# Kernel optimization log

Measured on AMD Instinct MI355X. Metric: run time of the kernel, lower is better.

Reference implementation:

```python
import jax, jax.numpy as jnp
import numpy as np

S = 8          # num_slots
DSLOT = 128    # slot_dim
D_IN = 768     # input feature dim
ITERS = 3      # slot_att_iter
RES = 21       # 336 // 16
NGRID = RES * RES   # 441 grid positions
NTOK = 441          # tokens kept per frame (no drop here)
NFRAME = 2
F_ = 2 * NFRAME + 1  # 5 frames per clip
CLIPS = 8
B = CLIPS * F_       # 40
SIGMA = 5.0
SCALE = DSLOT ** -0.5
EPS = 1e-8


def layernorm(x, g, b):
    m = x.mean(-1, keepdims=True)
    v = ((x - m) ** 2).mean(-1, keepdims=True)
    return (x - m) * jax.lax.rsqrt(v + 1e-5) * g + b


def setup_inputs() -> dict:
    key = jax.random.key(0)
    ks = iter(jax.random.split(key, 64))
    def nrm(shape, s=0.02):
        return jax.random.normal(next(ks), shape, jnp.float32) * s
    xs = jnp.linspace(-1.0, 1.0, RES)
    ys = jnp.linspace(-1.0, 1.0, RES)
    gx, gy = jnp.meshgrid(xs, ys)  # indexing='xy' as in torch
    abs_grid = jnp.stack([gx.ravel(), gy.ravel()], axis=-1)  # [NGRID, 2]
    return {
        "inputs": jax.random.normal(next(ks), (B, NTOK, D_IN), jnp.float32),
        "token_indices": jnp.sort(jax.random.randint(next(ks), (B, NTOK), 0, NGRID), axis=-1),
        "abs_grid": abs_grid,
        "slots_init": nrm((1, S, DSLOT), 0.1),
        "S_p_init": nrm((1, S, 1, 2), 0.02),
        "S_s_init": jax.random.uniform(next(ks), (1, S, 1, 2), jnp.float32, 0.3, 0.7),
        "WQ": nrm((DSLOT, DSLOT)), "ln_g": jnp.ones((DSLOT,)), "ln_b": jnp.zeros((DSLOT,)),
        "gru_w_ih": nrm((DSLOT, 3 * DSLOT)), "gru_w_hh": nrm((DSLOT, 3 * DSLOT)),
        "gru_b_ih": jnp.zeros((3 * DSLOT,)), "gru_b_hh": jnp.zeros((3 * DSLOT,)),
        "mlp_ln_g": jnp.ones((DSLOT,)), "mlp_ln_b": jnp.zeros((DSLOT,)),
        "mlp_w1": nrm((DSLOT, 4 * DSLOT)), "mlp_b1": jnp.zeros((4 * DSLOT,)),
        "mlp_w2": nrm((4 * DSLOT, DSLOT)), "mlp_b2": jnp.zeros((DSLOT,)),
        "WK": nrm((DSLOT, DSLOT)), "WV": nrm((DSLOT, DSLOT)),
        "Wg": nrm((2, DSLOT)), "bg": jnp.zeros((DSLOT,)),
        "Wf1": nrm((DSLOT, DSLOT)), "bf1": jnp.zeros((DSLOT,)),
        "Wf2": nrm((DSLOT, DSLOT)), "bf2": jnp.zeros((DSLOT,)),
        "im_ln1_g": jnp.ones((D_IN,)), "im_ln1_b": jnp.zeros((D_IN,)),
        "im_w1": nrm((D_IN, D_IN)), "im_b1": jnp.zeros((D_IN,)),
        "im_w2": nrm((D_IN, DSLOT)), "im_b2": jnp.zeros((DSLOT,)),
        "im_ln2_g": jnp.ones((DSLOT,)), "im_ln2_b": jnp.zeros((DSLOT,)),
        "fin_w": nrm((DSLOT, DSLOT)), "fin_b": jnp.zeros((DSLOT,)),
    }


def _forward(inputs, token_indices, abs_grid, slots_init, S_p_init, S_s_init,
             WQ, ln_g, ln_b, gru_w_ih, gru_w_hh, gru_b_ih, gru_b_hh,
             mlp_ln_g, mlp_ln_b, mlp_w1, mlp_b1, mlp_w2, mlp_b2,
             WK, WV, Wg, bg, Wf1, bf1, Wf2, bf2,
             im_ln1_g, im_ln1_b, im_w1, im_b1, im_w2, im_b2, im_ln2_g, im_ln2_b,
             fin_w, fin_b):
    Bb = inputs.shape[0]
    # initial_mlp: LN -> Linear -> ReLU -> Linear -> LN
    x = layernorm(inputs, im_ln1_g, im_ln1_b)
    x = jax.nn.relu(x @ im_w1 + im_b1)
    x = x @ im_w2 + im_b2
    x = layernorm(x, im_ln2_g, im_ln2_b)          # [B, N, Dslot]
    # K/V projections of inputs are slot-independent; compute once.
    Kx = x @ WK                                    # [B, N, Dslot]
    Vx = x @ WV
    ag = abs_grid[token_indices]                   # [B, N, 2] per-batch gather
    slots = jnp.broadcast_to(slots_init, (Bb, S, DSLOT))
    S_p = jnp.broadcast_to(S_p_init, (Bb, S, 1, 2))
    S_s = jnp.broadcast_to(S_s_init, (Bb, S, 1, 2))

    def f_net(z):  # f = Linear -> ReLU -> Linear
        return jax.nn.relu(z @ Wf1 + bf1) @ Wf2 + bf2

    attn = None
    for t in range(ITERS + 1):
        slots_prev = slots
        sn = layernorm(slots, ln_g, ln_b)
        rel = (ag[:, None] - S_p) / (S_s * SIGMA)  # [B, S, N, 2]
        gr = rel @ Wg + bg                          # [B, S, N, Dslot]
        k = f_net(Kx[:, None] + gr)
        v = f_net(Vx[:, None] + gr)
        q = sn @ WQ                                 # [B, S, Dslot]
        dots = jnp.einsum('bsd,bsjd->bsj', q, k) * SCALE
        attn = jax.nn.softmax(dots, axis=1) + EPS   # softmax over slots
        attn = attn / attn.sum(-1, keepdims=True)   # renormalize over tokens
        updates = jnp.einsum('bsjd,bsj->bsd', v, attn)
        S_p = jnp.einsum('bjd,bsj->bsd', ag, attn)[:, :, None, :]
        S_s = jnp.sqrt(jnp.einsum('bsjd,bsj->bsd', (ag[:, None] - S_p) ** 2, attn))[:, :, None, :]
        if t != ITERS:
            # torch GRUCell
            xg = updates.reshape(-1, DSLOT)
            hg = slots_prev.reshape(-1, DSLOT)
            gi = xg @ gru_w_ih + gru_b_ih
            gh = hg @ gru_w_hh + gru_b_hh
            i_r, i_z, i_n = jnp.split(gi, 3, axis=-1)
            h_r, h_z, h_n = jnp.split(gh, 3, axis=-1)
            r = jax.nn.sigmoid(i_r + h_r)
            z = jax.nn.sigmoid(i_z + h_z)
            n = jnp.tanh(i_n + r * h_n)
            slots = ((1.0 - z) * n + z * hg).reshape(Bb, S, DSLOT)
            # residual pre-LN MLP (dropout is identity in eval)
            y = layernorm(slots, mlp_ln_g, mlp_ln_b)
            y = jax.nn.relu(y @ mlp_w1 + mlp_b1) @ mlp_w2 + mlp_b2
            slots = slots + y
    slots = slots @ fin_w + fin_b
    attn_out = attn.reshape(-1, F_, S, NTOK)[:, NFRAME]  # center frame
    return slots, attn_out


def reference(inputs, token_indices, abs_grid, slots_init, S_p_init, S_s_init,
              WQ, ln_g, ln_b, gru_w_ih, gru_w_hh, gru_b_ih, gru_b_hh,
              mlp_ln_g, mlp_ln_b, mlp_w1, mlp_b1, mlp_w2, mlp_b2,
              WK, WV, Wg, bg, Wf1, bf1, Wf2, bf2,
              im_ln1_g, im_ln1_b, im_w1, im_b1, im_w2, im_b2, im_ln2_g, im_ln2_b,
              fin_w, fin_b):
    return _forward(inputs, token_indices, abs_grid, slots_init, S_p_init, S_s_init,
                    WQ, ln_g, ln_b, gru_w_ih, gru_w_hh, gru_b_ih, gru_b_hh,
                    mlp_ln_g, mlp_ln_b, mlp_w1, mlp_b1, mlp_w2, mlp_b2,
                    WK, WV, Wg, bg, Wf1, bf1, Wf2, bf2,
                    im_ln1_g, im_ln1_b, im_w1, im_b1, im_w2, im_b2, im_ln2_g, im_ln2_b,
                    fin_w, fin_b)
```

## Files before the change

### kernel.cpp

```cpp
#include <hip/hip_runtime.h>
#include <cstdio>

#define NB 40
#define NS 8
#define NT 441
#define DIN 768
#define DD 128
#define NTOT (NB*NT)
#define FSCALE 0.08838834764831843f

typedef short s8v __attribute__((ext_vector_type(8)));
typedef float f4v __attribute__((ext_vector_type(4)));

__device__ inline ushort f2bf(float f){
  unsigned u = __float_as_uint(f);
  unsigned r = (u + 0x7fffu + ((u >> 16) & 1u)) >> 16;
  return (ushort)r;
}
__device__ inline float bf2f(ushort h){ return __uint_as_float(((unsigned)h) << 16); }

struct PP {
  const float *inputs; const int *tok_idx; const float *abs_grid;
  const float *slots_init, *Sp_init, *Ss_init;
  const float *WQ, *ln_g, *ln_b;
  const float *gru_w_ih, *gru_w_hh, *gru_b_ih, *gru_b_hh;
  const float *mlp_ln_g, *mlp_ln_b, *mlp_w1, *mlp_b1, *mlp_w2, *mlp_b2;
  const float *WK, *WV, *Wg, *bg, *Wf1, *bf1, *Wf2, *bf2;
  const float *im_ln1_g, *im_ln1_b, *im_w1, *im_b1, *im_w2, *im_b2, *im_ln2_g, *im_ln2_b;
  const float *fin_w, *fin_b;
  float *x, *A_K, *A_V, *ag, *WKf, *WVf, *Wg1, *c1, *Wf2T;
  float *slots, *Sp0, *Sp1, *Ss0, *Ss1, *qW, *qb, *dots, *attn;
  float *hbar_part, *Sp_part, *hbar;
  ushort *xnh, *xnl, *hh, *hl, *W1Th, *W1Tl, *W2Th, *W2Tl;
  float *out;
};

__global__ __launch_bounds__(128) void prep_weights(PP p){
  int r = blockIdx.x, d = threadIdx.x;
  float accK = 0.f, accV = 0.f;
  for (int kk = 0; kk < DD; kk++){
    float w = p.Wf1[kk*DD + d];
    accK = fmaf(p.WK[r*DD+kk], w, accK);
    accV = fmaf(p.WV[r*DD+kk], w, accV);
  }
  p.WKf[r*DD+d] = accK; p.WVf[r*DD+d] = accV;
  if (r < 2){
    float a = 0.f;
    for (int kk = 0; kk < DD; kk++) a = fmaf(p.Wg[r*DD+kk], p.Wf1[kk*DD+d], a);
    p.Wg1[r*DD+d] = a;
  }
  if (r == 2){
    float a = 0.f;
    for (int kk = 0; kk < DD; kk++) a = fmaf(p.bg[kk], p.Wf1[kk*DD+d], a);
    p.c1[d] = a + p.bf1[d];
  }
  p.Wf2T[d*DD + r] = p.Wf2[r*DD + d];
}

__global__ __launch_bounds__(256) void transpose_split(const float* __restrict__ W,
                                                       ushort* __restrict__ WTh,
                                                       ushort* __restrict__ WTl,
                                                       int K, int N){
  __shared__ float tile[64][65];
  int tid = threadIdx.x;
  int k0 = blockIdx.x * 64, n0 = blockIdx.y * 64;
  #pragma unroll
  for (int i = 0; i < 4; i++){
    int k = i*16 + (tid >> 4);
    int n4 = (tid & 15) * 4;
    float4 v = *(const float4*)(W + (long)(k0+k)*N + n0 + n4);
    tile[k][n4+0] = v.x; tile[k][n4+1] = v.y; tile[k][n4+2] = v.z; tile[k][n4+3] = v.w;
  }
  __syncthreads();
  #pragma unroll
  for (int i = 0; i < 4; i++){
    int n = i*16 + (tid >> 4);
    int k4 = (tid & 15) * 4;
    ushort4 h4, l4;
    float v0 = tile[k4+0][n], v1 = tile[k4+1][n], v2 = tile[k4+2][n], v3 = tile[k4+3][n];
    h4.x = f2bf(v0); l4.x = f2bf(v0 - bf2f(h4.x));
    h4.y = f2bf(v1); l4.y = f2bf(v1 - bf2f(h4.y));
    h4.z = f2bf(v2); l4.z = f2bf(v2 - bf2f(h4.z));
    h4.w = f2bf(v3); l4.w = f2bf(v3 - bf2f(h4.w));
    *(ushort4*)(WTh + (long)(n0+n)*K + k0 + k4) = h4;
    *(ushort4*)(WTl + (long)(n0+n)*K + k0 + k4) = l4;
  }
}

__global__ __launch_bounds__(256) void ln1_split(PP p){
  int tok = blockIdx.x*4 + (threadIdx.x >> 6);
  int l = threadIdx.x & 63;
  const float* src = p.inputs + (long)tok*DIN;
  float4 v[3];
  float s = 0.f, s2 = 0.f;
  #pragma unroll
  for (int pp = 0; pp < 3; pp++){
    v[pp] = *(const float4*)(src + pp*256 + l*4);
    s  += v[pp].x + v[pp].y + v[pp].z + v[pp].w;
    s2 += v[pp].x*v[pp].x + v[pp].y*v[pp].y + v[pp].z*v[pp].z + v[pp].w*v[pp].w;
  }
  #pragma unroll
  for (int m = 1; m < 64; m <<= 1){ s += __shfl_xor(s, m); s2 += __shfl_xor(s2, m); }
  float mean = s*(1.f/DIN), var = s2*(1.f/DIN) - mean*mean;
  float rstd = rsqrtf(var + 1e-5f);
  #pragma unroll
  for (int pp = 0; pp < 3; pp++){
    int idx = pp*256 + l*4;
    float4 g = *(const float4*)(p.im_ln1_g + idx);
    float4 b = *(const float4*)(p.im_ln1_b + idx);
    float y0 = (v[pp].x-mean)*rstd*g.x + b.x;
    float y1 = (v[pp].y-mean)*rstd*g.y + b.y;
    float y2 = (v[pp].z-mean)*rstd*g.z + b.z;
    float y3 = (v[pp].w-mean)*rstd*g.w + b.w;
    ushort4 h4, l4;
    h4.x = f2bf(y0); l4.x = f2bf(y0 - bf2f(h4.x));
    h4.y = f2bf(y1); l4.y = f2bf(y1 - bf2f(h4.y));
    h4.z = f2bf(y2); l4.z = f2bf(y2 - bf2f(h4.z));
    h4.w = f2bf(y3); l4.w = f2bf(y3 - bf2f(h4.w));
    *(ushort4*)(p.xnh + (long)tok*DIN + idx) = h4;
    *(ushort4*)(p.xnl + (long)tok*DIN + idx) = l4;
  }
}

template<int EPI>
__global__ __launch_bounds__(256) void gemm_split(
    const ushort* __restrict__ Ah, const ushort* __restrict__ Al,
    const ushort* __restrict__ Bh, const ushort* __restrict__ Bl,
    const float* __restrict__ bias,
    ushort* __restrict__ Ch, ushort* __restrict__ Cl,
    float* __restrict__ Xout, const float* __restrict__ g2, const float* __restrict__ b2,
    int M)
{
  __shared__ __align__(16) char smem[64*132*4];
  ushort* As = (ushort*)smem;
  ushort* Bs = (ushort*)(smem + 10240);
  int tid = threadIdx.x;
  int n0 = blockIdx.x * 128, m0 = blockIdx.y * 64;
  int w = tid >> 6, lane = tid & 63;
  f4v acc[4][2];
  #pragma unroll
  for (int mf = 0; mf < 4; mf++)
    #pragma unroll
    for (int nf = 0; nf < 2; nf++) acc[mf][nf] = (f4v)(0.f);

  for (int kb = 0; kb < DIN; kb += 32){
    __syncthreads();
    #pragma unroll
    for (int i = 0; i < 2; i++){
      int c = tid + i*256;
      int s = c >> 8, r = (c >> 2) & 63, kg = c & 3;
      int gr = min(m0 + r, M-1);
      const float4 va = *(const float4*)((s ? Al : Ah) + (long)gr*DIN + kb + kg*8);
      *(float4*)(As + s*2560 + r*40 + kg*8) = va;
    }
    #pragma unroll
    for (int i = 0; i < 4; i++){
      int c = tid + i*256;
      int s = c >> 9, r = (c >> 2) & 127, kg = c & 3;
      const float4 vb = *(const float4*)((s ? Bl : Bh) + (long)(n0 + r)*DIN + kb + kg*8);
      *(float4*)(Bs + s*5120 + r*40 + kg*8) = vb;
    }
    __syncthreads();
    int kg = lane >> 4, rA = lane & 15;
    s8v a0[4], a1[4], b0[2], b1[2];
    #pragma unroll
    for (int mf = 0; mf < 4; mf++){
      a0[mf] = *(const s8v*)(As +        (mf*16 + rA)*40 + kg*8);
      a1[mf] = *(const s8v*)(As + 2560 + (mf*16 + rA)*40 + kg*8);
    }
    #pragma unroll
    for (int nf = 0; nf < 2; nf++){
      int rb = w*32 + nf*16 + rA;
      b0[nf] = *(const s8v*)(Bs +        rb*40 + kg*8);
      b1[nf] = *(const s8v*)(Bs + 5120 + rb*40 + kg*8);
    }
    #pragma unroll
    for (int mf = 0; mf < 4; mf++)
      #pragma unroll
      for (int nf = 0; nf < 2; nf++){
        acc[mf][nf] = __builtin_amdgcn_mfma_f32_16x16x32_bf16(a0[mf], b0[nf], acc[mf][nf], 0, 0, 0);
        acc[mf][nf] = __builtin_amdgcn_mfma_f32_16x16x32_bf16(a0[mf], b1[nf], acc[mf][nf], 0, 0, 0);
        acc[mf][nf] = __builtin_amdgcn_mfma_f32_16x16x32_bf16(a1[mf], b0[nf], acc[mf][nf], 0, 0, 0);
      }
  }

  int rbase = (lane >> 4) * 4, cn = lane & 15;
  if (EPI == 1){
    #pragma unroll
    for (int mf = 0; mf < 4; mf++)
      #pragma unroll
      for (int nf = 0; nf < 2; nf++){
        int n = n0 + w*32 + nf*16 + cn;
        float bs = bias[n];
        #pragma unroll
        for (int r = 0; r < 4; r++){
          int m = m0 + mf*16 + rbase + r;
          if (m < M){
            float v = fmaxf(acc[mf][nf][r] + bs, 0.f);
            ushort h = f2bf(v);
            Ch[(long)m*DIN + n] = h;
            Cl[(long)m*DIN + n] = f2bf(v - bf2f(h));
          }
        }
      }
  } else {
    __syncthreads();
    float* Dl = (float*)smem;
    #pragma unroll
    for (int mf = 0; mf < 4; mf++)
      #pragma unroll
      for (int nf = 0; nf < 2; nf++){
        int n = w*32 + nf*16 + cn;
        float bs = bias[n];
        #pragma unroll
        for (int r = 0; r < 4; r++)
          Dl[(mf*16 + rbase + r)*132 + n] = acc[mf][nf][r] + bs;
      }
    __syncthreads();
    for (int rr = 0; rr < 16; rr++){
      int row = w*16 + rr;
      float e0 = Dl[row*132 + lane], e1 = Dl[row*132 + 64 + lane];
      float s = e0 + e1, s2 = e0*e0 + e1*e1;
      #pragma unroll
      for (int m2 = 1; m2 < 64; m2 <<= 1){ s += __shfl_xor(s, m2); s2 += __shfl_xor(s2, m2); }
      float mean = s*(1.f/DD), var = s2*(1.f/DD) - mean*mean;
      float rstd = rsqrtf(var + 1e-5f);
      int m = m0 + row;
      if (m < M){
        Xout[(long)m*DD + lane]      = (e0-mean)*rstd*g2[lane]      + b2[lane];
        Xout[(long)m*DD + 64 + lane] = (e1-mean)*rstd*g2[64 + lane] + b2[64 + lane];
      }
    }
  }
}

__global__ void init_state(PP p){
  int i = blockIdx.x*256 + threadIdx.x;
  if (i < NB*NS*DD) p.slots[i] = p.slots_init[i & (NS*DD-1)];
  if (i < NB*NS*2){
    p.Sp0[i] = p.Sp_init[i & (NS*2-1)];
    p.Ss0[i] = p.Ss_init[i & (NS*2-1)];
  }
}

__global__ void gather_ag(PP p){
  int i = blockIdx.x*256 + threadIdx.x;
  if (i < NTOT){
    int idx = p.tok_idx[i];
    p.ag[i*2+0] = p.abs_grid[idx*2+0];
    p.ag[i*2+1] = p.abs_grid[idx*2+1];
  }
}

__global__ __launch_bounds__(256) void k2_proj(PP p){
  __shared__ float xt[32][132];
  int tid = threadIdx.x; int g0 = blockIdx.x * 32;
  for (int f = tid; f < 32*32; f += 256){
    int tok = f >> 5, pos = (f & 31) * 4;
    int gt = g0 + tok;
    float4 v = (gt < NTOT) ? *(const float4*)(p.x + (long)gt*DD + pos)
                           : make_float4(0.f,0.f,0.f,0.f);
    *(float4*)&xt[tok][pos] = v;
  }
  __syncthreads();
  int d = tid & 127, grp = tid >> 7;
  float aK[16], aV[16];
  float c1v = p.c1[d];
  #pragma unroll
  for (int t = 0; t < 16; t++){ aK[t] = c1v; aV[t] = c1v; }
  for (int kk = 0; kk < DD; kk += 4){
    float k0 = p.WKf[(kk+0)*DD+d], k1 = p.WKf[(kk+1)*DD+d], k2 = p.WKf[(kk+2)*DD+d], k3 = p.WKf[(kk+3)*DD+d];
    float v0 = p.WVf[(kk+0)*DD+d], v1 = p.WVf[(kk+1)*DD+d], v2 = p.WVf[(kk+2)*DD+d], v3 = p.WVf[(kk+3)*DD+d];
    #pragma unroll
    for (int t = 0; t < 16; t++){
      float4 xv = *(const float4*)&xt[grp*16+t][kk];
      aK[t] = fmaf(xv.x,k0, fmaf(xv.y,k1, fmaf(xv.z,k2, fmaf(xv.w,k3, aK[t]))));
      aV[t] = fmaf(xv.x,v0, fmaf(xv.y,v1, fmaf(xv.z,v2, fmaf(xv.w,v3, aV[t]))));
    }
  }
  #pragma unroll
  for (int t = 0; t < 16; t++){
    int gt = g0 + grp*16 + t;
    if (gt < NTOT){ p.A_K[(long)gt*DD+d] = aK[t]; p.A_V[(long)gt*DD+d] = aV[t]; }
  }
}

__global__ __launch_bounds__(128) void k3_slots(PP p){
  int bs = blockIdx.x, d = threadIdx.x;
  __shared__ float sn[128], q[128];
  __shared__ float rs[2][2];
  float v = p.slots[bs*DD+d];
  float s = v, s2 = v*v;
  for (int m = 1; m < 64; m <<= 1){ s += __shfl_xor(s, m); s2 += __shfl_xor(s2, m); }
  if ((d & 63) == 0){ rs[d>>6][0] = s; rs[d>>6][1] = s2; }
  __syncthreads();
  s = rs[0][0] + rs[1][0]; s2 = rs[0][1] + rs[1][1];
  float mean = s*(1.f/DD), var = s2*(1.f/DD) - mean*mean, rstd = rsqrtf(var + 1e-5f);
  sn[d] = (v-mean)*rstd*p.ln_g[d] + p.ln_b[d];
  __syncthreads();
  float acc = 0.f;
  for (int kk = 0; kk < DD; kk++) acc = fmaf(sn[kk], p.WQ[kk*DD+d], acc);
  q[d] = acc;
  __syncthreads();
  float a2 = 0.f;
  for (int dd = 0; dd < DD; dd++) a2 = fmaf(q[dd], p.Wf2T[dd*DD+d], a2);
  p.qW[bs*DD+d] = a2;
  float pb = p.bf2[d]*q[d];
  for (int m = 1; m < 64; m <<= 1) pb += __shfl_xor(pb, m);
  if ((d & 63) == 0) rs[d>>6][0] = pb;
  __syncthreads();
  if (d == 0) p.qb[bs] = (rs[0][0] + rs[1][0]) * FSCALE;
}

__global__ __launch_bounds__(256) void k4_dots(PP p, const float* Sp, const float* Ss){
  int b = blockIdx.x / 7, tile = blockIdx.x % 7;
  int tid = threadIdx.x, wid = tid >> 6, lane = tid & 63;
  int tl = lane >> 2, dg = lane & 3;
  __shared__ float qws[8][132];
  __shared__ float spss[8][4];
  __shared__ float qbs[8];
  for (int f = tid; f < 8*128; f += 256){
    int s = f >> 7, d = f & 127;
    qws[s][(d&31)*4 + (d>>5)] = p.qW[(b*NS+s)*DD+d];
  }
  if (tid < 8) qbs[tid] = p.qb[b*NS+tid];
  if (tid < 32){
    int s = tid >> 2, c = tid & 3;
    spss[s][c] = (c < 2) ? Sp[(b*NS+s)*2+c] : 1.f/(Ss[(b*NS+s)*2+(c-2)]*5.0f);
  }
  __syncthreads();
  int j = tile*64 + wid*16 + tl;
  bool valid = j < NT;
  int jj = valid ? j : 0;
  float aa[32], w0[32], w1[32];
  {
    const float* src = p.A_K + ((long)(b*NT+jj))*DD + dg*32;
    #pragma unroll
    for (int i4 = 0; i4 < 8; i4++){
      float4 t = *(const float4*)(src + i4*4);
      aa[i4*4+0]=t.x; aa[i4*4+1]=t.y; aa[i4*4+2]=t.z; aa[i4*4+3]=t.w;
    }
    #pragma unroll
    for (int i4 = 0; i4 < 8; i4++){
      float4 t0 = *(const float4*)(p.Wg1 + dg*32 + i4*4);
      float4 t1 = *(const float4*)(p.Wg1 + DD + dg*32 + i4*4);
      w0[i4*4+0]=t0.x; w0[i4*4+1]=t0.y; w0[i4*4+2]=t0.z; w0[i4*4+3]=t0.w;
      w1[i4*4+0]=t1.x; w1[i4*4+1]=t1.y; w1[i4*4+2]=t1.z; w1[i4*4+3]=t1.w;
    }
  }
  float ag0 = p.ag[(b*NT+jj)*2], ag1 = p.ag[(b*NT+jj)*2+1];
  #pragma unroll
  for (int s = 0; s < 8; s++){
    float rel0 = (ag0 - spss[s][0])*spss[s][2];
    float rel1 = (ag1 - spss[s][1])*spss[s][3];
    float acc = 0.f;
    #pragma unroll
    for (int i = 0; i < 32; i++){
      float hk = fmaxf(fmaf(rel0, w0[i], fmaf(rel1, w1[i], aa[i])), 0.f);
      acc = fmaf(hk, qws[s][i*4+dg], acc);
    }
    acc += __shfl_xor(acc, 1); acc += __shfl_xor(acc, 2);
    if (dg == 0 && valid) p.dots[(b*NS+s)*NT + j] = acc*FSCALE + qbs[s];
  }
}

__global__ __launch_bounds__(256) void k5_softmax(PP p){
  int b = blockIdx.x, tid = threadIdx.x;
  float a0[8], a1[8];
  float psum[8];
  #pragma unroll
  for (int s = 0; s < 8; s++) psum[s] = 0.f;
  bool has1 = (tid + 256) < NT;
  {
    int j = tid;
    float dv[8]; float m = -1e30f;
    #pragma unroll
    for (int s = 0; s < 8; s++){ dv[s] = p.dots[(b*NS+s)*NT+j]; m = fmaxf(m, dv[s]); }
    float tot = 0.f;
    #pragma unroll
    for (int s = 0; s < 8; s++){ dv[s] = expf(dv[s]-m); tot += dv[s]; }
    float inv = 1.f/tot;
    #pragma unroll
    for (int s = 0; s < 8; s++){ a0[s] = dv[s]*inv + 1e-8f; psum[s] += a0[s]; }
  }
  if (has1){
    int j = tid + 256;
    float dv[8]; float m = -1e30f;
    #pragma unroll
    for (int s = 0; s < 8; s++){ dv[s] = p.dots[(b*NS+s)*NT+j]; m = fmaxf(m, dv[s]); }
    float tot = 0.f;
    #pragma unroll
    for (int s = 0; s < 8; s++){ dv[s] = expf(dv[s]-m); tot += dv[s]; }
    float inv = 1.f/tot;
    #pragma unroll
    for (int s = 0; s < 8; s++){ a1[s] = dv[s]*inv + 1e-8f; psum[s] += a1[s]; }
  }
  #pragma unroll
  for (int s = 0; s < 8; s++)
    for (int m2 = 1; m2 < 64; m2 <<= 1) psum[s] += __shfl_xor(psum[s], m2);
  __shared__ float wsum[4][8];
  __shared__ float sums[8];
  if ((tid & 63) == 0)
    for (int s = 0; s < 8; s++) wsum[tid>>6][s] = psum[s];
  __syncthreads();
  if (tid < 8) sums[tid] = wsum[0][tid]+wsum[1][tid]+wsum[2][tid]+wsum[3][tid];
  __syncthreads();
  {
    int j = tid;
    #pragma unroll
    for (int s = 0; s < 8; s++) p.attn[(b*NS+s)*NT+j] = a0[s]/sums[s];
  }
  if (has1){
    int j = tid + 256;
    #pragma unroll
    for (int s = 0; s < 8; s++) p.attn[(b*NS+s)*NT+j] = a1[s]/sums[s];
  }
}

__global__ __launch_bounds__(256) void k6a(PP p, const float* Sp, const float* Ss){
  int b = blockIdx.x >> 3, tile = blockIdx.x & 7;
  int tid = threadIdx.x, wid = tid >> 6, lane = tid & 63;
  int j0 = tile*56; int jn = min(NT, j0+56) - j0;
  __shared__ float atile[8][56];
  __shared__ float spss[8][4];
  __shared__ float hpart[4][8][128];
  __shared__ float ppart[4][8][2];
  for (int f = tid; f < 8*56; f += 256){
    int s = f/56, jj = f%56;
    atile[s][jj] = (j0+jj < NT) ? p.attn[(b*NS+s)*NT + j0+jj] : 0.f;
  }
  if (tid < 32){
    int s = tid >> 2, c = tid & 3;
    spss[s][c] = (c < 2) ? Sp[(b*NS+s)*2+c] : 1.f/(Ss[(b*NS+s)*2+(c-2)]*5.0f);
  }
  __syncthreads();
  int d0 = lane, d1 = lane + 64;
  float wg00 = p.Wg1[d0], wg10 = p.Wg1[DD+d0], wg01 = p.Wg1[d1], wg11 = p.Wg1[DD+d1];
  float acc0[8], acc1[8], accp[8];
  #pragma unroll
  for (int s = 0; s < 8; s++){ acc0[s]=0.f; acc1[s]=0.f; accp[s]=0.f; }
  int cpar = lane & 1;
  for (int jj = wid; jj < jn; jj += 4){
    int j = j0 + jj;
    float av0 = p.A_V[((long)(b*NT+j))*DD + d0];
    float av1 = p.A_V[((long)(b*NT+j))*DD + d1];
    float ag0 = p.ag[(b*NT+j)*2], ag1 = p.ag[(b*NT+j)*2+1];
    float agc = cpar ? ag1 : ag0;
    #pragma unroll
    for (int s = 0; s < 8; s++){
      float rel0 = (ag0 - spss[s][0])*spss[s][2];
      float rel1 = (ag1 - spss[s][1])*spss[s][3];
      float a = atile[s][jj];
      float hv0 = fmaxf(fmaf(rel0,wg00, fmaf(rel1,wg10, av0)), 0.f);
      float hv1 = fmaxf(fmaf(rel0,wg01, fmaf(rel1,wg11, av1)), 0.f);
      acc0[s] = fmaf(a, hv0, acc0[s]);
      acc1[s] = fmaf(a, hv1, acc1[s]);
      if (lane < 2) accp[s] = fmaf(a, agc, accp[s]);
    }
  }
  #pragma unroll
  for (int s = 0; s < 8; s++){ hpart[wid][s][d0] = acc0[s]; hpart[wid][s][d1] = acc1[s]; }
  if (lane < 2)
    for (int s = 0; s < 8; s++) ppart[wid][s][lane] = accp[s];
  __syncthreads();
  for (int f = tid; f < 8*128; f += 256){
    int s = f >> 7, d = f & 127;
    p.hbar_part[((b*8+tile)*NS+s)*DD+d] = hpart[0][s][d]+hpart[1][s][d]+hpart[2][s][d]+hpart[3][s][d];
  }
  if (tid < 16){
    int s = tid >> 1, c = tid & 1;
    p.Sp_part[((b*8+tile)*NS+s)*2+c] = ppart[0][s][c]+ppart[1][s][c]+ppart[2][s][c]+ppart[3][s][c];
  }
}

__global__ __launch_bounds__(128) void k6r(PP p, float* Sp_new, float* Ss_new){
  int bs = blockIdx.x; int b = bs >> 3, s = bs & 7, d = threadIdx.x;
  float v = 0.f;
  for (int t = 0; t < 8; t++) v += p.hbar_part[((b*8+t)*NS+s)*DD+d];
  p.hbar[bs*DD+d] = v;
  __shared__ float spl[2];
  if (d < 2){
    float u = 0.f;
    for (int t = 0; t < 8; t++) u += p.Sp_part[((b*8+t)*NS+s)*2+d];
    Sp_new[bs*2+d] = u; spl[d] = u;
  }
  __syncthreads();
  float sp0 = spl[0], sp1 = spl[1];
  float q0 = 0.f, q1 = 0.f;
  for (int j = d; j < NT; j += 128){
    float at = p.attn[bs*NT+j];
    float e0 = p.ag[(b*NT+j)*2]   - sp0;
    float e1 = p.ag[(b*NT+j)*2+1] - sp1;
    q0 = fmaf(at, e0*e0, q0); q1 = fmaf(at, e1*e1, q1);
  }
  for (int m = 1; m < 64; m <<= 1){ q0 += __shfl_xor(q0, m); q1 += __shfl_xor(q1, m); }
  __shared__ float rr[2][2];
  if ((d & 63) == 0){ rr[d>>6][0] = q0; rr[d>>6][1] = q1; }
  __syncthreads();
  if (d == 0){
    Ss_new[bs*2+0] = sqrtf(rr[0][0]+rr[1][0]);
    Ss_new[bs*2+1] = sqrtf(rr[0][1]+rr[1][1]);
  }
}

__global__ __launch_bounds__(128) void k7_update(PP p){
  int bs = blockIdx.x, d = threadIdx.x;
  __shared__ float hb[128], upd[128], hprev[128], y[128], h1[512];
  __shared__ float rr[2][2];
  hb[d] = p.hbar[bs*DD+d]; hprev[d] = p.slots[bs*DD+d];
  __syncthreads();
  float a = p.bf2[d];
  for (int kk = 0; kk < DD; kk++) a = fmaf(hb[kk], p.Wf2[kk*DD+d], a);
  upd[d] = a;
  __syncthreads();
  float gi[3], gh[3];
  #pragma unroll
  for (int i = 0; i < 3; i++){ gi[i] = p.gru_b_ih[d+128*i]; gh[i] = p.gru_b_hh[d+128*i]; }
  for (int kk = 0; kk < DD; kk++){
    float xv = upd[kk], hv = hprev[kk];
    #pragma unroll
    for (int i = 0; i < 3; i++){
      gi[i] = fmaf(xv, p.gru_w_ih[kk*384 + d+128*i], gi[i]);
      gh[i] = fmaf(hv, p.gru_w_hh[kk*384 + d+128*i], gh[i]);
    }
  }
  float r = 1.f/(1.f+expf(-(gi[0]+gh[0])));
  float z = 1.f/(1.f+expf(-(gi[1]+gh[1])));
  float n = tanhf(gi[2] + r*gh[2]);
  float hnew = (1.f-z)*n + z*hprev[d];
  float s = hnew, s2 = hnew*hnew;
  for (int m = 1; m < 64; m <<= 1){ s += __shfl_xor(s, m); s2 += __shfl_xor(s2, m); }
  if ((d & 63) == 0){ rr[d>>6][0] = s; rr[d>>6][1] = s2; }
  __syncthreads();
  s = rr[0][0]+rr[1][0]; s2 = rr[0][1]+rr[1][1];
  float mean = s*(1.f/DD), var = s2*(1.f/DD)-mean*mean, rstd = rsqrtf(var+1e-5f);
  y[d] = (hnew-mean)*rstd*p.mlp_ln_g[d] + p.mlp_ln_b[d];
  __syncthreads();
  #pragma unroll
  for (int i = 0; i < 4; i++){
    int o = d + 128*i;
    float acc = p.mlp_b1[o];
    for (int kk = 0; kk < DD; kk++) acc = fmaf(y[kk], p.mlp_w1[kk*512+o], acc);
    h1[o] = fmaxf(acc, 0.f);
  }
  __syncthreads();
  float acc2 = p.mlp_b2[d];
  for (int o = 0; o < 512; o++) acc2 = fmaf(h1[o], p.mlp_w2[o*DD+d], acc2);
  p.slots[bs*DD+d] = hnew + acc2;
}

__global__ __launch_bounds__(128) void k8_final(PP p){
  int bs = blockIdx.x, d = threadIdx.x;
  __shared__ float sl[128];
  sl[d] = p.slots[bs*DD+d];
  __syncthreads();
  float a = p.fin_b[d];
  for (int kk = 0; kk < DD; kk++) a = fmaf(sl[kk], p.fin_w[kk*DD+d], a);
  p.out[bs*DD+d] = a;
}

__global__ void k8_attn(PP p){
  int i = blockIdx.x*256 + threadIdx.x;
  if (i < 8*NS*NT){
    int clip = i / (NS*NT);
    int rem  = i % (NS*NT);
    int b = clip*5 + 2;
    p.out[NB*NS*DD + i] = p.attn[b*NS*NT + rem];
  }
}

extern "C" void kernel_launch(void* const* d_in, const int* in_sizes, int n_in,
                              void* d_out, int out_size, void* d_ws, size_t ws_size,
                              hipStream_t stream){
  PP p;
  p.inputs=(const float*)d_in[0]; p.tok_idx=(const int*)d_in[1]; p.abs_grid=(const float*)d_in[2];
  p.slots_init=(const float*)d_in[3]; p.Sp_init=(const float*)d_in[4]; p.Ss_init=(const float*)d_in[5];
  p.WQ=(const float*)d_in[6]; p.ln_g=(const float*)d_in[7]; p.ln_b=(const float*)d_in[8];
  p.gru_w_ih=(const float*)d_in[9]; p.gru_w_hh=(const float*)d_in[10];
  p.gru_b_ih=(const float*)d_in[11]; p.gru_b_hh=(const float*)d_in[12];
  p.mlp_ln_g=(const float*)d_in[13]; p.mlp_ln_b=(const float*)d_in[14];
  p.mlp_w1=(const float*)d_in[15]; p.mlp_b1=(const float*)d_in[16];
  p.mlp_w2=(const float*)d_in[17]; p.mlp_b2=(const float*)d_in[18];
  p.WK=(const float*)d_in[19]; p.WV=(const float*)d_in[20]; p.Wg=(const float*)d_in[21]; p.bg=(const float*)d_in[22];
  p.Wf1=(const float*)d_in[23]; p.bf1=(const float*)d_in[24]; p.Wf2=(const float*)d_in[25]; p.bf2=(const float*)d_in[26];
  p.im_ln1_g=(const float*)d_in[27]; p.im_ln1_b=(const float*)d_in[28];
  p.im_w1=(const float*)d_in[29]; p.im_b1=(const float*)d_in[30];
  p.im_w2=(const float*)d_in[31]; p.im_b2=(const float*)d_in[32];
  p.im_ln2_g=(const float*)d_in[33]; p.im_ln2_b=(const float*)d_in[34];
  p.fin_w=(const float*)d_in[35]; p.fin_b=(const float*)d_in[36];

  float* w = (float*)d_ws;
  size_t need = 0;
  auto alloc = [&](size_t nfl){ nfl = (nfl + 3) & ~(size_t)3; float* r = w + need; need += nfl; return r; };
  p.x    = alloc((size_t)NTOT*DD);
  p.A_K  = alloc((size_t)NTOT*DD);
  p.A_V  = alloc((size_t)NTOT*DD);
  p.ag   = alloc((size_t)NTOT*2);
  p.WKf  = alloc(DD*DD);
  p.WVf  = alloc(DD*DD);
  p.Wg1  = alloc(2*DD);
  p.c1   = alloc(DD);
  p.Wf2T = alloc(DD*DD);
  p.slots= alloc(NB*NS*DD);
  p.Sp0  = alloc(NB*NS*2);
  p.Sp1  = alloc(NB*NS*2);
  p.Ss0  = alloc(NB*NS*2);
  p.Ss1  = alloc(NB*NS*2);
  p.qW   = alloc(NB*NS*DD);
  p.qb   = alloc(NB*NS);
  p.dots = alloc((size_t)NB*NS*NT);
  p.attn = alloc((size_t)NB*NS*NT);
  p.hbar_part = alloc((size_t)NB*8*NS*DD);
  p.Sp_part   = alloc((size_t)NB*8*NS*2);
  p.hbar = alloc(NB*NS*DD);
  p.xnh  = (ushort*)alloc((size_t)NTOT*DIN/2);
  p.xnl  = (ushort*)alloc((size_t)NTOT*DIN/2);
  p.hh   = (ushort*)alloc((size_t)NTOT*DIN/2);
  p.hl   = (ushort*)alloc((size_t)NTOT*DIN/2);
  p.W1Th = (ushort*)alloc((size_t)DIN*DIN/2);
  p.W1Tl = (ushort*)alloc((size_t)DIN*DIN/2);
  p.W2Th = (ushort*)alloc((size_t)DD*DIN/2);
  p.W2Tl = (ushort*)alloc((size_t)DD*DIN/2);
  p.out = (float*)d_out;
  if (ws_size < need*sizeof(float)){
    fprintf(stderr, "kernel_launch: ws too small (%zu < %zu)\n", ws_size, need*sizeof(float));
    return;
  }

  prep_weights<<<dim3(DD), dim3(DD), 0, stream>>>(p);
  transpose_split<<<dim3(DIN/64, DIN/64), dim3(256), 0, stream>>>(p.im_w1, p.W1Th, p.W1Tl, DIN, DIN);
  transpose_split<<<dim3(DIN/64, DD/64), dim3(256), 0, stream>>>(p.im_w2, p.W2Th, p.W2Tl, DIN, DD);
  init_state<<<dim3((NB*NS*DD+255)/256), dim3(256), 0, stream>>>(p);
  gather_ag<<<dim3((NTOT+255)/256), dim3(256), 0, stream>>>(p);
  ln1_split<<<dim3(NTOT/4), dim3(256), 0, stream>>>(p);
  gemm_split<1><<<dim3(DIN/128, (NTOT+63)/64), dim3(256), 0, stream>>>(
      p.xnh, p.xnl, p.W1Th, p.W1Tl, p.im_b1, p.hh, p.hl,
      nullptr, nullptr, nullptr, NTOT);
  gemm_split<2><<<dim3(1, (NTOT+63)/64), dim3(256), 0, stream>>>(
      p.hh, p.hl, p.W2Th, p.W2Tl, p.im_b2, nullptr, nullptr,
      p.x, p.im_ln2_g, p.im_ln2_b, NTOT);
  k2_proj<<<dim3((NTOT+31)/32), dim3(256), 0, stream>>>(p);

  float* Sp[2] = {p.Sp0, p.Sp1};
  float* Ss[2] = {p.Ss0, p.Ss1};
  int cur = 0;
  for (int t = 0; t < 4; t++){
    k3_slots<<<dim3(NB*NS), dim3(128), 0, stream>>>(p);
    k4_dots<<<dim3(NB*7), dim3(256), 0, stream>>>(p, Sp[cur], Ss[cur]);
    k5_softmax<<<dim3(NB), dim3(256), 0, stream>>>(p);
    if (t < 3){
      k6a<<<dim3(NB*8), dim3(256), 0, stream>>>(p, Sp[cur], Ss[cur]);
      k6r<<<dim3(NB*NS), dim3(128), 0, stream>>>(p, Sp[cur^1], Ss[cur^1]);
      k7_update<<<dim3(NB*NS), dim3(128), 0, stream>>>(p);
      cur ^= 1;
    }
  }
  k8_final<<<dim3(NB*NS), dim3(128), 0, stream>>>(p);
  k8_attn<<<dim3((8*NS*NT+255)/256), dim3(256), 0, stream>>>(p);
}
```

Baseline: 477.3 us.

## Fuse slot-attention iteration loop into one persistent per-batch kernel

Replaces the roughly 20 small per-iteration launches (slot LN/query, dots, softmax, weighted aggregation, reductions, GRU/MLP update, final projection) with a single kernel of one 512-thread block per batch element. All iteration state stays in shared memory, and the token grid gather and state init are folded in. Weight matrices are pre-transposed so each lane reads contiguous float4 rows. This removes launch overhead and global round-trips of intermediates, but only 40 blocks run on a large GPU, so per-batch work is serialized within one CU.

```diff
diff --git a/kernel.cpp b/kernel.cpp
--- a/kernel.cpp
+++ b/kernel.cpp
@@ -4,6 +4,7 @@
 #define NB 40
 #define NS 8
 #define NT 441
+#define NTP 448
 #define DIN 768
 #define DD 128
 #define NTOT (NB*NT)
@@ -18,6 +19,9 @@
   return (ushort)r;
 }
 __device__ inline float bf2f(ushort h){ return __uint_as_float(((unsigned)h) << 16); }
+__device__ inline float dot4(float4 a, float4 b){
+  return fmaf(a.x,b.x, fmaf(a.y,b.y, fmaf(a.z,b.z, a.w*b.w)));
+}
 
 struct PP {
   const float *inputs; const int *tok_idx; const float *abs_grid;
@@ -28,9 +32,8 @@
   const float *WK, *WV, *Wg, *bg, *Wf1, *bf1, *Wf2, *bf2;
   const float *im_ln1_g, *im_ln1_b, *im_w1, *im_b1, *im_w2, *im_b2, *im_ln2_g, *im_ln2_b;
   const float *fin_w, *fin_b;
-  float *x, *A_K, *A_V, *ag, *WKf, *WVf, *Wg1, *c1, *Wf2T;
-  float *slots, *Sp0, *Sp1, *Ss0, *Ss1, *qW, *qb, *dots, *attn;
-  float *hbar_part, *Sp_part, *hbar;
+  float *x, *A_K, *A_V, *WKf, *WVf, *Wg1, *c1, *Wf2T;
+  float *WQT, *gihT, *ghhT, *w1T, *w2T, *finT;
   ushort *xnh, *xnl, *hh, *hl, *W1Th, *W1Tl, *W2Th, *W2Tl;
   float *out;
 };
@@ -55,6 +58,21 @@
     p.c1[d] = a + p.bf1[d];
   }
   p.Wf2T[d*DD + r] = p.Wf2[r*DD + d];
+}
+
+__global__ __launch_bounds__(256) void prep_transposes(PP p){
+  long i = (long)blockIdx.x*256 + threadIdx.x;
+  if (i < 16384){ int r = i >> 7, c = i & 127; p.WQT[c*128 + r] = p.WQ[i]; return; }
+  i -= 16384;
+  if (i < 49152){ int r = i / 384, c = i % 384; p.gihT[c*128 + r] = p.gru_w_ih[i]; return; }
+  i -= 49152;
+  if (i < 49152){ int r = i / 384, c = i % 384; p.ghhT[c*128 + r] = p.gru_w_hh[i]; return; }
+  i -= 49152;
+  if (i < 65536){ int r = i / 512, c = i % 512; p.w1T[c*128 + r] = p.mlp_w1[i]; return; }
+  i -= 65536;
+  if (i < 65536){ int r = i / 128, c = i % 128; p.w2T[c*512 + r] = p.mlp_w2[i]; return; }
+  i -= 65536;
+  { int r = i >> 7, c = i & 127; p.finT[c*128 + r] = p.fin_w[i]; }
 }
 
 __global__ __launch_bounds__(256) void transpose_split(const float* __restrict__ W,
@@ -234,24 +252,6 @@
   }
 }
 
-__global__ void init_state(PP p){
-  int i = blockIdx.x*256 + threadIdx.x;
-  if (i < NB*NS*DD) p.slots[i] = p.slots_init[i & (NS*DD-1)];
-  if (i < NB*NS*2){
-    p.Sp0[i] = p.Sp_init[i & (NS*2-1)];
-    p.Ss0[i] = p.Ss_init[i & (NS*2-1)];
-  }
-}
-
-__global__ void gather_ag(PP p){
-  int i = blockIdx.x*256 + threadIdx.x;
-  if (i < NTOT){
-    int idx = p.tok_idx[i];
-    p.ag[i*2+0] = p.abs_grid[idx*2+0];
-    p.ag[i*2+1] = p.abs_grid[idx*2+1];
-  }
-}
-
 __global__ __launch_bounds__(256) void k2_proj(PP p){
   __shared__ float xt[32][132];
   int tid = threadIdx.x; int g0 = blockIdx.x * 32;
@@ -285,287 +285,333 @@
   }
 }
 
-__global__ __launch_bounds__(128) void k3_slots(PP p){
-  int bs = blockIdx.x, d = threadIdx.x;
-  __shared__ float sn[128], q[128];
-  __shared__ float rs[2][2];
-  float v = p.slots[bs*DD+d];
-  float s = v, s2 = v*v;
-  for (int m = 1; m < 64; m <<= 1){ s += __shfl_xor(s, m); s2 += __shfl_xor(s2, m); }
-  if ((d & 63) == 0){ rs[d>>6][0] = s; rs[d>>6][1] = s2; }
+__global__ __launch_bounds__(512) void k_iter(PP p){
+  const int b = blockIdx.x;
+  const int tid = threadIdx.x;
+  const int wid = tid >> 6, lane = tid & 63;
+
+  __shared__ float slots_s[8][128];
+  __shared__ float sns[8][128];
+  __shared__ float qs[8][128];
+  __shared__ float ys[8][128];
+  __shared__ float hbar_s[8][128];
+  __shared__ float upds[8][128];
+  __shared__ float qws[8][132];
+  __shared__ float qbs[8];
+  __shared__ float spss[8][4];
+  __shared__ float Sp_c[8][2], Ss_c[8][2];
+  __shared__ float agl[NTP][2];
+  __shared__ float wg01[2][128];
+  __shared__ float red[8][16];
+  __shared__ float sums[8];
+  __shared__ float u_a[4096];
+  __shared__ float u_b[4096];
+
+  for (int f = tid; f < NS*DD; f += 512) slots_s[f>>7][f&127] = p.slots_init[f];
+  if (tid < 16){ Sp_c[tid>>1][tid&1] = p.Sp_init[tid]; Ss_c[tid>>1][tid&1] = p.Ss_init[tid]; }
+  for (int f = tid; f < NT; f += 512){
+    int idx = p.tok_idx[b*NT + f];
+    agl[f][0] = p.abs_grid[idx*2+0];
+    agl[f][1] = p.abs_grid[idx*2+1];
+  }
+  if (tid < 256) wg01[tid>>7][tid&127] = p.Wg1[tid];
   __syncthreads();
-  s = rs[0][0] + rs[1][0]; s2 = rs[0][1] + rs[1][1];
-  float mean = s*(1.f/DD), var = s2*(1.f/DD) - mean*mean, rstd = rsqrtf(var + 1e-5f);
-  sn[d] = (v-mean)*rstd*p.ln_g[d] + p.ln_b[d];
-  __syncthreads();
-  float acc = 0.f;
-  for (int kk = 0; kk < DD; kk++) acc = fmaf(sn[kk], p.WQ[kk*DD+d], acc);
-  q[d] = acc;
-  __syncthreads();
-  float a2 = 0.f;
-  for (int dd = 0; dd < DD; dd++) a2 = fmaf(q[dd], p.Wf2T[dd*DD+d], a2);
-  p.qW[bs*DD+d] = a2;
-  float pb = p.bf2[d]*q[d];
-  for (int m = 1; m < 64; m <<= 1) pb += __shfl_xor(pb, m);
-  if ((d & 63) == 0) rs[d>>6][0] = pb;
-  __syncthreads();
-  if (d == 0) p.qb[bs] = (rs[0][0] + rs[1][0]) * FSCALE;
-}
-
-__global__ __launch_bounds__(256) void k4_dots(PP p, const float* Sp, const float* Ss){
-  int b = blockIdx.x / 7, tile = blockIdx.x % 7;
-  int tid = threadIdx.x, wid = tid >> 6, lane = tid & 63;
-  int tl = lane >> 2, dg = lane & 3;
-  __shared__ float qws[8][132];
-  __shared__ float spss[8][4];
-  __shared__ float qbs[8];
-  for (int f = tid; f < 8*128; f += 256){
-    int s = f >> 7, d = f & 127;
-    qws[s][(d&31)*4 + (d>>5)] = p.qW[(b*NS+s)*DD+d];
-  }
-  if (tid < 8) qbs[tid] = p.qb[b*NS+tid];
-  if (tid < 32){
-    int s = tid >> 2, c = tid & 3;
-    spss[s][c] = (c < 2) ? Sp[(b*NS+s)*2+c] : 1.f/(Ss[(b*NS+s)*2+(c-2)]*5.0f);
-  }
-  __syncthreads();
-  int j = tile*64 + wid*16 + tl;
-  bool valid = j < NT;
-  int jj = valid ? j : 0;
-  float aa[32], w0[32], w1[32];
+
+  for (int t = 0; t < 4; t++){
+    {
+      int s = wid;
+      float v0 = slots_s[s][lane], v1 = slots_s[s][lane+64];
+      float sm = v0+v1, sq = v0*v0 + v1*v1;
+      #pragma unroll
+      for (int m = 1; m < 64; m <<= 1){ sm += __shfl_xor(sm, m); sq += __shfl_xor(sq, m); }
+      float mean = sm*(1.f/DD), var = sq*(1.f/DD) - mean*mean;
+      float rstd = rsqrtf(var + 1e-5f);
+      float sn0 = (v0-mean)*rstd*p.ln_g[lane]    + p.ln_b[lane];
+      float sn1 = (v1-mean)*rstd*p.ln_g[lane+64] + p.ln_b[lane+64];
+      sns[s][lane] = sn0; sns[s][lane+64] = sn1;
+      __syncthreads();
+      float q0 = 0.f, q1 = 0.f;
+      for (int k4 = 0; k4 < 32; k4++){
+        float4 sv  = *(const float4*)&sns[s][k4*4];
+        float4 wa  = *(const float4*)(p.WQT + (long)lane*128      + k4*4);
+        float4 wb  = *(const float4*)(p.WQT + (long)(lane+64)*128 + k4*4);
+        q0 += dot4(sv, wa); q1 += dot4(sv, wb);
+      }
+      qs[s][lane] = q0; qs[s][lane+64] = q1;
+      __syncthreads();
+      float a0 = 0.f, a1 = 0.f;
+      for (int k4 = 0; k4 < 32; k4++){
+        float4 qv = *(const float4*)&qs[s][k4*4];
+        float4 wa = *(const float4*)(p.Wf2 + (long)lane*128      + k4*4);
+        float4 wb = *(const float4*)(p.Wf2 + (long)(lane+64)*128 + k4*4);
+        a0 += dot4(qv, wa); a1 += dot4(qv, wb);
+      }
+      qws[s][(lane&31)*4 + (lane>>5)] = a0;
+      int d1 = lane + 64;
+      qws[s][(d1&31)*4 + (d1>>5)] = a1;
+      float pb = p.bf2[lane]*q0 + p.bf2[d1]*q1;
+      #pragma unroll
+      for (int m = 1; m < 64; m <<= 1) pb += __shfl_xor(pb, m);
+      if (lane == 0) qbs[s] = pb * FSCALE;
+      if (lane < 4) spss[s][lane] = (lane < 2) ? Sp_c[s][lane] : 1.f/(Ss_c[s][lane-2]*5.0f);
+      __syncthreads();
+    }
+
+    {
+      int jl = tid >> 2, dg = tid & 3;
+      float w0[32], w1[32];
+      #pragma unroll
+      for (int i = 0; i < 32; i++){ w0[i] = wg01[0][dg*32+i]; w1[i] = wg01[1][dg*32+i]; }
+      float sp0[8], sp1[8], si0[8], si1[8];
+      #pragma unroll
+      for (int s = 0; s < 8; s++){
+        sp0[s]=spss[s][0]; sp1[s]=spss[s][1]; si0[s]=spss[s][2]; si1[s]=spss[s][3];
+      }
+      for (int jp = 0; jp < 4; jp++){
+        int j = jp*128 + jl;
+        bool valid = j < NT;
+        int jj = valid ? j : 0;
+        const float* src = p.A_K + ((long)(b*NT+jj))*DD + dg*32;
+        float aa[32];
+        #pragma unroll
+        for (int i4 = 0; i4 < 8; i4++){
+          float4 tt = *(const float4*)(src + i4*4);
+          aa[i4*4+0]=tt.x; aa[i4*4+1]=tt.y; aa[i4*4+2]=tt.z; aa[i4*4+3]=tt.w;
+        }
+        float g0 = agl[jj][0], g1 = agl[jj][1];
+        #pragma unroll
+        for (int s = 0; s < 8; s++){
+          float rel0 = (g0 - sp0[s])*si0[s];
+          float rel1 = (g1 - sp1[s])*si1[s];
+          float acc = 0.f;
+          #pragma unroll
+          for (int i = 0; i < 32; i++){
+            float hk = fmaxf(fmaf(rel0, w0[i], fmaf(rel1, w1[i], aa[i])), 0.f);
+            acc = fmaf(hk, qws[s][i*4+dg], acc);
+          }
+          acc += __shfl_xor(acc, 1); acc += __shfl_xor(acc, 2);
+          if (dg == 0 && valid) u_a[s*NTP + j] = acc*FSCALE + qbs[s];
+        }
+      }
+      __syncthreads();
+    }
+
+    {
+      int j = tid; bool jv = j < NT;
+      float a[8];
+      float psum[8];
+      if (jv){
+        float dv[8]; float m = -1e30f;
+        #pragma unroll
+        for (int s = 0; s < 8; s++){ dv[s] = u_a[s*NTP+j]; m = fmaxf(m, dv[s]); }
+        float tot = 0.f;
+        #pragma unroll
+        for (int s = 0; s < 8; s++){ dv[s] = expf(dv[s]-m); tot += dv[s]; }
+        float inv = 1.f/tot;
+        #pragma unroll
+        for (int s = 0; s < 8; s++){ a[s] = dv[s]*inv + 1e-8f; }
+      } else {
+        #pragma unroll
+        for (int s = 0; s < 8; s++) a[s] = 0.f;
+      }
+      #pragma unroll
+      for (int s = 0; s < 8; s++){
+        psum[s] = a[s];
+        #pragma unroll
+        for (int m2 = 1; m2 < 64; m2 <<= 1) psum[s] += __shfl_xor(psum[s], m2);
+      }
+      if (lane == 0){
+        #pragma unroll
+        for (int s = 0; s < 8; s++) red[wid][s] = psum[s];
+      }
+      __syncthreads();
+      if (tid < 8){
+        float tsum = 0.f;
+        #pragma unroll
+        for (int w2 = 0; w2 < 8; w2++) tsum += red[w2][tid];
+        sums[tid] = tsum;
+      }
+      __syncthreads();
+      float g0 = jv ? agl[j][0] : 0.f, g1 = jv ? agl[j][1] : 0.f;
+      float av[8];
+      #pragma unroll
+      for (int s = 0; s < 8; s++){
+        av[s] = a[s]/sums[s];
+        if (jv) u_b[s*NTP + j] = av[s];
+      }
+      if (t < 3){
+        float spp[16];
+        #pragma unroll
+        for (int s = 0; s < 8; s++){ spp[s*2] = av[s]*g0; spp[s*2+1] = av[s]*g1; }
+        #pragma unroll
+        for (int k = 0; k < 16; k++){
+          #pragma unroll
+          for (int m2 = 1; m2 < 64; m2 <<= 1) spp[k] += __shfl_xor(spp[k], m2);
+        }
+        if (lane == 0){
+          #pragma unroll
+          for (int k = 0; k < 16; k++) red[wid][k] = spp[k];
+        }
+        __syncthreads();
+        if (tid < 16){
+          float tt = 0.f;
+          #pragma unroll
+          for (int w2 = 0; w2 < 8; w2++) tt += red[w2][tid];
+          Sp_c[tid>>1][tid&1] = tt;
+        }
+        __syncthreads();
+        float qq[16];
+        #pragma unroll
+        for (int s = 0; s < 8; s++){
+          float e0 = g0 - Sp_c[s][0], e1 = g1 - Sp_c[s][1];
+          float q0v = av[s]*e0*e0, q1v = av[s]*e1*e1;
+          qq[s*2]   = jv ? q0v : 0.f;
+          qq[s*2+1] = jv ? q1v : 0.f;
+        }
+        #pragma unroll
+        for (int k = 0; k < 16; k++){
+          #pragma unroll
+          for (int m2 = 1; m2 < 64; m2 <<= 1) qq[k] += __shfl_xor(qq[k], m2);
+        }
+        if (lane == 0){
+          #pragma unroll
+          for (int k = 0; k < 16; k++) red[wid][k] = qq[k];
+        }
+        __syncthreads();
+        if (tid < 16){
+          float tt = 0.f;
+          #pragma unroll
+          for (int w2 = 0; w2 < 8; w2++) tt += red[w2][tid];
+          Ss_c[tid>>1][tid&1] = sqrtf(tt);
+        }
+        __syncthreads();
+      } else {
+        if ((b % 5) == 2 && jv){
+          long base = (long)NB*NS*DD + (long)(b/5)*NS*NT;
+          #pragma unroll
+          for (int s = 0; s < 8; s++) p.out[base + s*NT + j] = av[s];
+        }
+        __syncthreads();
+      }
+    }
+
+    if (t < 3){
+      {
+        int d = tid & 127, jg = tid >> 7;
+        float wgd0 = wg01[0][d], wgd1 = wg01[1][d];
+        float sp0[8], sp1[8], si0[8], si1[8];
+        #pragma unroll
+        for (int s = 0; s < 8; s++){
+          sp0[s]=spss[s][0]; sp1[s]=spss[s][1]; si0[s]=spss[s][2]; si1[s]=spss[s][3];
+        }
+        float acc[8];
+        #pragma unroll
+        for (int s = 0; s < 8; s++) acc[s] = 0.f;
+        for (int jj = jg; jj < NT; jj += 4){
+          float avv = p.A_V[((long)(b*NT+jj))*DD + d];
+          float g0 = agl[jj][0], g1 = agl[jj][1];
+          #pragma unroll
+          for (int s = 0; s < 8; s++){
+            float rel0 = (g0 - sp0[s])*si0[s];
+            float rel1 = (g1 - sp1[s])*si1[s];
+            float hv = fmaxf(fmaf(rel0, wgd0, fmaf(rel1, wgd1, avv)), 0.f);
+            acc[s] = fmaf(u_b[s*NTP + jj], hv, acc[s]);
+          }
+        }
+        #pragma unroll
+        for (int s = 0; s < 8; s++) u_a[jg*1024 + s*128 + d] = acc[s];
+        __syncthreads();
+        for (int f = tid; f < 1024; f += 512){
+          int s = f >> 7, dd = f & 127;
+          hbar_s[s][dd] = u_a[s*128+dd] + u_a[1024 + s*128+dd] + u_a[2048 + s*128+dd] + u_a[3072 + s*128+dd];
+        }
+        __syncthreads();
+      }
+
+      {
+        int s = wid, d0 = lane, d1 = lane + 64;
+        float u0 = p.bf2[d0], u1 = p.bf2[d1];
+        for (int k4 = 0; k4 < 32; k4++){
+          float4 hb = *(const float4*)&hbar_s[s][k4*4];
+          float4 wa = *(const float4*)(p.Wf2T + (long)d0*128 + k4*4);
+          float4 wb = *(const float4*)(p.Wf2T + (long)d1*128 + k4*4);
+          u0 += dot4(hb, wa); u1 += dot4(hb, wb);
+        }
+        upds[s][d0] = u0; upds[s][d1] = u1;
+        __syncthreads();
+        float gia[3], gib[3], gha[3], ghb[3];
+        #pragma unroll
+        for (int i = 0; i < 3; i++){
+          gia[i] = p.gru_b_ih[d0+128*i]; gib[i] = p.gru_b_ih[d1+128*i];
+          gha[i] = p.gru_b_hh[d0+128*i]; ghb[i] = p.gru_b_hh[d1+128*i];
+        }
+        for (int k4 = 0; k4 < 32; k4++){
+          float4 xv = *(const float4*)&upds[s][k4*4];
+          float4 hv = *(const float4*)&slots_s[s][k4*4];
+          #pragma unroll
+          for (int i = 0; i < 3; i++){
+            float4 wia = *(const float4*)(p.gihT + (long)(d0+128*i)*128 + k4*4);
+            float4 wib = *(const float4*)(p.gihT + (long)(d1+128*i)*128 + k4*4);
+            float4 wha = *(const float4*)(p.ghhT + (long)(d0+128*i)*128 + k4*4);
+            float4 whb = *(const float4*)(p.ghhT + (long)(d1+128*i)*128 + k4*4);
+            gia[i] += dot4(xv, wia); gib[i] += dot4(xv, wib);
+            gha[i] += dot4(hv, wha); ghb[i] += dot4(hv, whb);
+          }
+        }
+        float hp0 = slots_s[s][d0], hp1 = slots_s[s][d1];
+        float r0 = 1.f/(1.f+expf(-(gia[0]+gha[0])));
+        float z0 = 1.f/(1.f+expf(-(gia[1]+gha[1])));
+        float n0 = tanhf(gia[2] + r0*gha[2]);
+        float hn0 = (1.f-z0)*n0 + z0*hp0;
+        float r1 = 1.f/(1.f+expf(-(gib[0]+ghb[0])));
+        float z1 = 1.f/(1.f+expf(-(gib[1]+ghb[1])));
+        float n1 = tanhf(gib[2] + r1*ghb[2]);
+        float hn1 = (1.f-z1)*n1 + z1*hp1;
+        float sm = hn0+hn1, sq = hn0*hn0 + hn1*hn1;
+        #pragma unroll
+        for (int m = 1; m < 64; m <<= 1){ sm += __shfl_xor(sm, m); sq += __shfl_xor(sq, m); }
+        float mean = sm*(1.f/DD), var = sq*(1.f/DD) - mean*mean;
+        float rstd = rsqrtf(var + 1e-5f);
+        ys[s][d0] = (hn0-mean)*rstd*p.mlp_ln_g[d0] + p.mlp_ln_b[d0];
+        ys[s][d1] = (hn1-mean)*rstd*p.mlp_ln_g[d1] + p.mlp_ln_b[d1];
+        __syncthreads();
+        #pragma unroll
+        for (int i = 0; i < 8; i++){
+          int o = i*64 + lane;
+          float acc = p.mlp_b1[o];
+          for (int k4 = 0; k4 < 32; k4++){
+            float4 yv = *(const float4*)&ys[s][k4*4];
+            float4 wv = *(const float4*)(p.w1T + (long)o*128 + k4*4);
+            acc += dot4(yv, wv);
+          }
+          u_b[s*512 + o] = fmaxf(acc, 0.f);
+        }
+        __syncthreads();
+        float a0 = p.mlp_b2[d0], a1 = p.mlp_b2[d1];
+        for (int o4 = 0; o4 < 128; o4++){
+          float4 hvv = *(const float4*)&u_b[s*512 + o4*4];
+          float4 wa = *(const float4*)(p.w2T + (long)d0*512 + o4*4);
+          float4 wb = *(const float4*)(p.w2T + (long)d1*512 + o4*4);
+          a0 += dot4(hvv, wa); a1 += dot4(hvv, wb);
+        }
+        slots_s[s][d0] = hn0 + a0;
+        slots_s[s][d1] = hn1 + a1;
+        __syncthreads();
+      }
+    }
+  }
+
   {
-    const float* src = p.A_K + ((long)(b*NT+jj))*DD + dg*32;
-    #pragma unroll
-    for (int i4 = 0; i4 < 8; i4++){
-      float4 t = *(const float4*)(src + i4*4);
-      aa[i4*4+0]=t.x; aa[i4*4+1]=t.y; aa[i4*4+2]=t.z; aa[i4*4+3]=t.w;
-    }
-    #pragma unroll
-    for (int i4 = 0; i4 < 8; i4++){
-      float4 t0 = *(const float4*)(p.Wg1 + dg*32 + i4*4);
-      float4 t1 = *(const float4*)(p.Wg1 + DD + dg*32 + i4*4);
-      w0[i4*4+0]=t0.x; w0[i4*4+1]=t0.y; w0[i4*4+2]=t0.z; w0[i4*4+3]=t0.w;
-      w1[i4*4+0]=t1.x; w1[i4*4+1]=t1.y; w1[i4*4+2]=t1.z; w1[i4*4+3]=t1.w;
-    }
-  }
-  float ag0 = p.ag[(b*NT+jj)*2], ag1 = p.ag[(b*NT+jj)*2+1];
-  #pragma unroll
-  for (int s = 0; s < 8; s++){
-    float rel0 = (ag0 - spss[s][0])*spss[s][2];
-    float rel1 = (ag1 - spss[s][1])*spss[s][3];
-    float acc = 0.f;
-    #pragma unroll
-    for (int i = 0; i < 32; i++){
-      float hk = fmaxf(fmaf(rel0, w0[i], fmaf(rel1, w1[i], aa[i])), 0.f);
-      acc = fmaf(hk, qws[s][i*4+dg], acc);
-    }
-    acc += __shfl_xor(acc, 1); acc += __shfl_xor(acc, 2);
-    if (dg == 0 && valid) p.dots[(b*NS+s)*NT + j] = acc*FSCALE + qbs[s];
-  }
-}
-
-__global__ __launch_bounds__(256) void k5_softmax(PP p){
-  int b = blockIdx.x, tid = threadIdx.x;
-  float a0[8], a1[8];
-  float psum[8];
-  #pragma unroll
-  for (int s = 0; s < 8; s++) psum[s] = 0.f;
-  bool has1 = (tid + 256) < NT;
-  {
-    int j = tid;
-    float dv[8]; float m = -1e30f;
-    #pragma unroll
-    for (int s = 0; s < 8; s++){ dv[s] = p.dots[(b*NS+s)*NT+j]; m = fmaxf(m, dv[s]); }
-    float tot = 0.f;
-    #pragma unroll
-    for (int s = 0; s < 8; s++){ dv[s] = expf(dv[s]-m); tot += dv[s]; }
-    float inv = 1.f/tot;
-    #pragma unroll
-    for (int s = 0; s < 8; s++){ a0[s] = dv[s]*inv + 1e-8f; psum[s] += a0[s]; }
-  }
-  if (has1){
-    int j = tid + 256;
-    float dv[8]; float m = -1e30f;
-    #pragma unroll
-    for (int s = 0; s < 8; s++){ dv[s] = p.dots[(b*NS+s)*NT+j]; m = fmaxf(m, dv[s]); }
-    float tot = 0.f;
-    #pragma unroll
-    for (int s = 0; s < 8; s++){ dv[s] = expf(dv[s]-m); tot += dv[s]; }
-    float inv = 1.f/tot;
-    #pragma unroll
-    for (int s = 0; s < 8; s++){ a1[s] = dv[s]*inv + 1e-8f; psum[s] += a1[s]; }
-  }
-  #pragma unroll
-  for (int s = 0; s < 8; s++)
-    for (int m2 = 1; m2 < 64; m2 <<= 1) psum[s] += __shfl_xor(psum[s], m2);
-  __shared__ float wsum[4][8];
-  __shared__ float sums[8];
-  if ((tid & 63) == 0)
-    for (int s = 0; s < 8; s++) wsum[tid>>6][s] = psum[s];
-  __syncthreads();
-  if (tid < 8) sums[tid] = wsum[0][tid]+wsum[1][tid]+wsum[2][tid]+wsum[3][tid];
-  __syncthreads();
-  {
-    int j = tid;
-    #pragma unroll
-    for (int s = 0; s < 8; s++) p.attn[(b*NS+s)*NT+j] = a0[s]/sums[s];
-  }
-  if (has1){
-    int j = tid + 256;
-    #pragma unroll
-    for (int s = 0; s < 8; s++) p.attn[(b*NS+s)*NT+j] = a1[s]/sums[s];
-  }
-}
-
-__global__ __launch_bounds__(256) void k6a(PP p, const float* Sp, const float* Ss){
-  int b = blockIdx.x >> 3, tile = blockIdx.x & 7;
-  int tid = threadIdx.x, wid = tid >> 6, lane = tid & 63;
-  int j0 = tile*56; int jn = min(NT, j0+56) - j0;
-  __shared__ float atile[8][56];
-  __shared__ float spss[8][4];
-  __shared__ float hpart[4][8][128];
-  __shared__ float ppart[4][8][2];
-  for (int f = tid; f < 8*56; f += 256){
-    int s = f/56, jj = f%56;
-    atile[s][jj] = (j0+jj < NT) ? p.attn[(b*NS+s)*NT + j0+jj] : 0.f;
-  }
-  if (tid < 32){
-    int s = tid >> 2, c = tid & 3;
-    spss[s][c] = (c < 2) ? Sp[(b*NS+s)*2+c] : 1.f/(Ss[(b*NS+s)*2+(c-2)]*5.0f);
-  }
-  __syncthreads();
-  int d0 = lane, d1 = lane + 64;
-  float wg00 = p.Wg1[d0], wg10 = p.Wg1[DD+d0], wg01 = p.Wg1[d1], wg11 = p.Wg1[DD+d1];
-  float acc0[8], acc1[8], accp[8];
-  #pragma unroll
-  for (int s = 0; s < 8; s++){ acc0[s]=0.f; acc1[s]=0.f; accp[s]=0.f; }
-  int cpar = lane & 1;
-  for (int jj = wid; jj < jn; jj += 4){
-    int j = j0 + jj;
-    float av0 = p.A_V[((long)(b*NT+j))*DD + d0];
-    float av1 = p.A_V[((long)(b*NT+j))*DD + d1];
-    float ag0 = p.ag[(b*NT+j)*2], ag1 = p.ag[(b*NT+j)*2+1];
-    float agc = cpar ? ag1 : ag0;
-    #pragma unroll
-    for (int s = 0; s < 8; s++){
-      float rel0 = (ag0 - spss[s][0])*spss[s][2];
-      float rel1 = (ag1 - spss[s][1])*spss[s][3];
-      float a = atile[s][jj];
-      float hv0 = fmaxf(fmaf(rel0,wg00, fmaf(rel1,wg10, av0)), 0.f);
-      float hv1 = fmaxf(fmaf(rel0,wg01, fmaf(rel1,wg11, av1)), 0.f);
-      acc0[s] = fmaf(a, hv0, acc0[s]);
-      acc1[s] = fmaf(a, hv1, acc1[s]);
-      if (lane < 2) accp[s] = fmaf(a, agc, accp[s]);
-    }
-  }
-  #pragma unroll
-  for (int s = 0; s < 8; s++){ hpart[wid][s][d0] = acc0[s]; hpart[wid][s][d1] = acc1[s]; }
-  if (lane < 2)
-    for (int s = 0; s < 8; s++) ppart[wid][s][lane] = accp[s];
-  __syncthreads();
-  for (int f = tid; f < 8*128; f += 256){
-    int s = f >> 7, d = f & 127;
-    p.hbar_part[((b*8+tile)*NS+s)*DD+d] = hpart[0][s][d]+hpart[1][s][d]+hpart[2][s][d]+hpart[3][s][d];
-  }
-  if (tid < 16){
-    int s = tid >> 1, c = tid & 1;
-    p.Sp_part[((b*8+tile)*NS+s)*2+c] = ppart[0][s][c]+ppart[1][s][c]+ppart[2][s][c]+ppart[3][s][c];
-  }
-}
-
-__global__ __launch_bounds__(128) void k6r(PP p, float* Sp_new, float* Ss_new){
-  int bs = blockIdx.x; int b = bs >> 3, s = bs & 7, d = threadIdx.x;
-  float v = 0.f;
-  for (int t = 0; t < 8; t++) v += p.hbar_part[((b*8+t)*NS+s)*DD+d];
-  p.hbar[bs*DD+d] = v;
-  __shared__ float spl[2];
-  if (d < 2){
-    float u = 0.f;
-    for (int t = 0; t < 8; t++) u += p.Sp_part[((b*8+t)*NS+s)*2+d];
-    Sp_new[bs*2+d] = u; spl[d] = u;
-  }
-  __syncthreads();
-  float sp0 = spl[0], sp1 = spl[1];
-  float q0 = 0.f, q1 = 0.f;
-  for (int j = d; j < NT; j += 128){
-    float at = p.attn[bs*NT+j];
-    float e0 = p.ag[(b*NT+j)*2]   - sp0;
-    float e1 = p.ag[(b*NT+j)*2+1] - sp1;
-    q0 = fmaf(at, e0*e0, q0); q1 = fmaf(at, e1*e1, q1);
-  }
-  for (int m = 1; m < 64; m <<= 1){ q0 += __shfl_xor(q0, m); q1 += __shfl_xor(q1, m); }
-  __shared__ float rr[2][2];
-  if ((d & 63) == 0){ rr[d>>6][0] = q0; rr[d>>6][1] = q1; }
-  __syncthreads();
-  if (d == 0){
-    Ss_new[bs*2+0] = sqrtf(rr[0][0]+rr[1][0]);
-    Ss_new[bs*2+1] = sqrtf(rr[0][1]+rr[1][1]);
-  }
-}
-
-__global__ __launch_bounds__(128) void k7_update(PP p){
-  int bs = blockIdx.x, d = threadIdx.x;
-  __shared__ float hb[128], upd[128], hprev[128], y[128], h1[512];
-  __shared__ float rr[2][2];
-  hb[d] = p.hbar[bs*DD+d]; hprev[d] = p.slots[bs*DD+d];
-  __syncthreads();
-  float a = p.bf2[d];
-  for (int kk = 0; kk < DD; kk++) a = fmaf(hb[kk], p.Wf2[kk*DD+d], a);
-  upd[d] = a;
-  __syncthreads();
-  float gi[3], gh[3];
-  #pragma unroll
-  for (int i = 0; i < 3; i++){ gi[i] = p.gru_b_ih[d+128*i]; gh[i] = p.gru_b_hh[d+128*i]; }
-  for (int kk = 0; kk < DD; kk++){
-    float xv = upd[kk], hv = hprev[kk];
-    #pragma unroll
-    for (int i = 0; i < 3; i++){
-      gi[i] = fmaf(xv, p.gru_w_ih[kk*384 + d+128*i], gi[i]);
-      gh[i] = fmaf(hv, p.gru_w_hh[kk*384 + d+128*i], gh[i]);
-    }
-  }
-  float r = 1.f/(1.f+expf(-(gi[0]+gh[0])));
-  float z = 1.f/(1.f+expf(-(gi[1]+gh[1])));
-  float n = tanhf(gi[2] + r*gh[2]);
-  float hnew = (1.f-z)*n + z*hprev[d];
-  float s = hnew, s2 = hnew*hnew;
-  for (int m = 1; m < 64; m <<= 1){ s += __shfl_xor(s, m); s2 += __shfl_xor(s2, m); }
-  if ((d & 63) == 0){ rr[d>>6][0] = s; rr[d>>6][1] = s2; }
-  __syncthreads();
-  s = rr[0][0]+rr[1][0]; s2 = rr[0][1]+rr[1][1];
-  float mean = s*(1.f/DD), var = s2*(1.f/DD)-mean*mean, rstd = rsqrtf(var+1e-5f);
-  y[d] = (hnew-mean)*rstd*p.mlp_ln_g[d] + p.mlp_ln_b[d];
-  __syncthreads();
-  #pragma unroll
-  for (int i = 0; i < 4; i++){
-    int o = d + 128*i;
-    float acc = p.mlp_b1[o];
-    for (int kk = 0; kk < DD; kk++) acc = fmaf(y[kk], p.mlp_w1[kk*512+o], acc);
-    h1[o] = fmaxf(acc, 0.f);
-  }
-  __syncthreads();
-  float acc2 = p.mlp_b2[d];
-  for (int o = 0; o < 512; o++) acc2 = fmaf(h1[o], p.mlp_w2[o*DD+d], acc2);
-  p.slots[bs*DD+d] = hnew + acc2;
-}
-
-__global__ __launch_bounds__(128) void k8_final(PP p){
-  int bs = blockIdx.x, d = threadIdx.x;
-  __shared__ float sl[128];
-  sl[d] = p.slots[bs*DD+d];
-  __syncthreads();
-  float a = p.fin_b[d];
-  for (int kk = 0; kk < DD; kk++) a = fmaf(sl[kk], p.fin_w[kk*DD+d], a);
-  p.out[bs*DD+d] = a;
-}
-
-__global__ void k8_attn(PP p){
-  int i = blockIdx.x*256 + threadIdx.x;
-  if (i < 8*NS*NT){
-    int clip = i / (NS*NT);
-    int rem  = i % (NS*NT);
-    int b = clip*5 + 2;
-    p.out[NB*NS*DD + i] = p.attn[b*NS*NT + rem];
+    int s = wid, d0 = lane, d1 = lane + 64;
+    float a0 = p.fin_b[d0], a1 = p.fin_b[d1];
+    for (int k4 = 0; k4 < 32; k4++){
+      float4 sl = *(const float4*)&slots_s[s][k4*4];
+      float4 wa = *(const float4*)(p.finT + (long)d0*128 + k4*4);
+      float4 wb = *(const float4*)(p.finT + (long)d1*128 + k4*4);
+      a0 += dot4(sl, wa); a1 += dot4(sl, wb);
+    }
+    p.out[(long)(b*NS + s)*DD + d0] = a0;
+    p.out[(long)(b*NS + s)*DD + d1] = a1;
   }
 }
 
@@ -595,24 +641,17 @@
   p.x    = alloc((size_t)NTOT*DD);
   p.A_K  = alloc((size_t)NTOT*DD);
   p.A_V  = alloc((size_t)NTOT*DD);
-  p.ag   = alloc((size_t)NTOT*2);
   p.WKf  = alloc(DD*DD);
   p.WVf  = alloc(DD*DD);
   p.Wg1  = alloc(2*DD);
   p.c1   = alloc(DD);
   p.Wf2T = alloc(DD*DD);
-  p.slots= alloc(NB*NS*DD);
-  p.Sp0  = alloc(NB*NS*2);
-  p.Sp1  = alloc(NB*NS*2);
-  p.Ss0  = alloc(NB*NS*2);
-  p.Ss1  = alloc(NB*NS*2);
-  p.qW   = alloc(NB*NS*DD);
-  p.qb   = alloc(NB*NS);
-  p.dots = alloc((size_t)NB*NS*NT);
-  p.attn = alloc((size_t)NB*NS*NT);
-  p.hbar_part = alloc((size_t)NB*8*NS*DD);
-  p.Sp_part   = alloc((size_t)NB*8*NS*2);
-  p.hbar = alloc(NB*NS*DD);
+  p.WQT  = alloc(DD*DD);
+  p.gihT = alloc(3*DD*DD);
+  p.ghhT = alloc(3*DD*DD);
+  p.w1T  = alloc(4*DD*DD);
+  p.w2T  = alloc(4*DD*DD);
+  p.finT = alloc(DD*DD);
   p.xnh  = (ushort*)alloc((size_t)NTOT*DIN/2);
   p.xnl  = (ushort*)alloc((size_t)NTOT*DIN/2);
   p.hh   = (ushort*)alloc((size_t)NTOT*DIN/2);
@@ -627,11 +666,10 @@
     return;
   }
 
-  prep_weights<<<dim3(DD), dim3(DD), 0, stream>>>(p);
+  prep_weights<<<dim3(DD), dim3(128), 0, stream>>>(p);
+  prep_transposes<<<dim3(1024), dim3(256), 0, stream>>>(p);
   transpose_split<<<dim3(DIN/64, DIN/64), dim3(256), 0, stream>>>(p.im_w1, p.W1Th, p.W1Tl, DIN, DIN);
   transpose_split<<<dim3(DIN/64, DD/64), dim3(256), 0, stream>>>(p.im_w2, p.W2Th, p.W2Tl, DIN, DD);
-  init_state<<<dim3((NB*NS*DD+255)/256), dim3(256), 0, stream>>>(p);
-  gather_ag<<<dim3((NTOT+255)/256), dim3(256), 0, stream>>>(p);
   ln1_split<<<dim3(NTOT/4), dim3(256), 0, stream>>>(p);
   gemm_split<1><<<dim3(DIN/128, (NTOT+63)/64), dim3(256), 0, stream>>>(
       p.xnh, p.xnl, p.W1Th, p.W1Tl, p.im_b1, p.hh, p.hl,
@@ -640,21 +678,5 @@
       p.hh, p.hl, p.W2Th, p.W2Tl, p.im_b2, nullptr, nullptr,
       p.x, p.im_ln2_g, p.im_ln2_b, NTOT);
   k2_proj<<<dim3((NTOT+31)/32), dim3(256), 0, stream>>>(p);
-
-  float* Sp[2] = {p.Sp0, p.Sp1};
-  float* Ss[2] = {p.Ss0, p.Ss1};
-  int cur = 0;
-  for (int t = 0; t < 4; t++){
-    k3_slots<<<dim3(NB*NS), dim3(128), 0, stream>>>(p);
-    k4_dots<<<dim3(NB*7), dim3(256), 0, stream>>>(p, Sp[cur], Ss[cur]);
-    k5_softmax<<<dim3(NB), dim3(256), 0, stream>>>(p);
-    if (t < 3){
-      k6a<<<dim3(NB*8), dim3(256), 0, stream>>>(p, Sp[cur], Ss[cur]);
-      k6r<<<dim3(NB*NS), dim3(128), 0, stream>>>(p, Sp[cur^1], Ss[cur^1]);
-      k7_update<<<dim3(NB*NS), dim3(128), 0, stream>>>(p);
-      cur ^= 1;
-    }
-  }
-  k8_final<<<dim3(NB*NS), dim3(128), 0, stream>>>(p);
-  k8_attn<<<dim3((8*NS*NT+255)/256), dim3(256), 0, stream>>>(p);
-}
+  k_iter<<<dim3(NB), dim3(512), 0, stream>>>(p);
+}
```

New measurement: 1.461 ms. +206.0%, slower.
